# Kernel tuning notes

Hardware: AMD Instinct MI355X
Metric: run time of the kernel (lower is better)

The kernel has to match this reference:

```python
import jax, jax.numpy as jnp
import numpy as np

# Static problem sizes (uniform complexes so the per-complex torch loop vectorizes)
B, P, L = 8, 512, 64          # complexes, protein atoms/complex, ligand atoms/complex
H, RB = 128, 32               # hidden_dim, radial_bins
CUTOFF = 8.0
NPT, NLT = 20, 16             # atom-type vocab sizes


def _linear_init(k, din, dout):
    s = 1.0 / np.sqrt(din)
    kw, kb = jax.random.split(k)
    W = jax.random.uniform(kw, (din, dout), minval=-s, maxval=s, dtype=jnp.float32)
    b = jax.random.uniform(kb, (dout,), minval=-s, maxval=s, dtype=jnp.float32)
    return W, b


def setup_inputs() -> dict:
    key = jax.random.key(0)
    ks = jax.random.split(key, 12)
    # positions spread over ~a pocket-sized box so the cutoff mask is non-trivial
    protein_pos = jax.random.normal(ks[0], (B * P, 3), dtype=jnp.float32) * 4.0
    ligand_pos = jax.random.normal(ks[1], (B * L, 3), dtype=jnp.float32) * 4.0
    protein_atom_type = jax.random.randint(ks[2], (B * P,), 0, NPT)
    ligand_atom_type = jax.random.randint(ks[3], (B * L,), 0, NLT)
    protein_batch = jnp.repeat(jnp.arange(B), P)
    ligand_batch = jnp.repeat(jnp.arange(B), L)
    prot_emb = jax.random.normal(ks[4], (NPT, H), dtype=jnp.float32)
    lig_emb = jax.random.normal(ks[5], (NLT, H), dtype=jnp.float32)
    W1, b1 = _linear_init(ks[6], 2 * H + RB, H)
    W2, b2 = _linear_init(ks[7], H, H)
    W3, b3 = _linear_init(ks[8], H, H)
    Wr1, br1 = _linear_init(ks[9], H, H)
    Wr2, br2 = _linear_init(ks[10], H, 1)
    return dict(protein_pos=protein_pos, ligand_pos=ligand_pos,
                prot_emb=prot_emb, lig_emb=lig_emb,
                W1=W1, b1=b1, W2=W2, b2=b2, W3=W3, b3=b3,
                Wr1=Wr1, br1=br1, Wr2=Wr2, br2=br2,
                protein_atom_type=protein_atom_type, ligand_atom_type=ligand_atom_type,
                protein_batch=protein_batch, ligand_batch=ligand_batch)


def reference(protein_pos, ligand_pos, prot_emb, lig_emb,
              W1, b1, W2, b2, W3, b3, Wr1, br1, Wr2, br2,
              protein_atom_type, ligand_atom_type, protein_batch, ligand_batch):
    # batches are contiguous with uniform P/L atoms per complex -> reshape to [B, ., .]
    pos_p = protein_pos.reshape(B, P, 3)
    pos_l = ligand_pos.reshape(B, L, 3)
    hp = prot_emb[protein_atom_type].reshape(B, P, H)
    hl = lig_emb[ligand_atom_type].reshape(B, L, H)

    diff = pos_p[:, :, None, :] - pos_l[:, None, :, :]          # [B,P,L,3]
    dist = jnp.linalg.norm(diff, axis=-1)                        # [B,P,L]
    mask = dist < CUTOFF                                         # [B,P,L]

    centers = jnp.linspace(0.0, CUTOFF, RB, dtype=dist.dtype)    # radial_centers buffer
    width = jnp.asarray(0.5 * CUTOFF / RB, dtype=dist.dtype)     # radial_width buffer
    rb = jnp.exp(-0.5 * ((dist[..., None] - centers) / (width + 1e-8)) ** 2)  # [B,P,L,RB]

    pair = jnp.concatenate([
        jnp.broadcast_to(hp[:, :, None, :], (B, P, L, H)),
        jnp.broadcast_to(hl[:, None, :, :], (B, P, L, H)),
        rb,
    ], axis=-1)                                                  # [B,P,L,2H+RB]

    h = jax.nn.relu(pair @ W1 + b1)
    h = jax.nn.relu(h @ W2 + b2)
    h = jax.nn.relu(h @ W3 + b3)                                 # [B,P,L,H]

    m = mask[..., None].astype(h.dtype)
    cnt = jnp.sum(mask, axis=(1, 2)).astype(h.dtype)             # valid pairs per complex
    complex_repr = jnp.sum(h * m, axis=(1, 2)) / jnp.maximum(cnt, 1.0)[:, None]  # [B,H]

    score = jax.nn.relu(complex_repr @ Wr1 + br1) @ Wr2 + br2    # [B,1]
    score = jnp.where(cnt[:, None] > 0, score, 0.0)              # torch emits 0 if no pairs
    return score[:, 0]                                           # [B]
```

## Files before the change

kernel.cpp:

```cpp
#include <hip/hip_runtime.h>
#include <hip/hip_bf16.h>
#include <math.h>

#define NB 8
#define NP 512
#define NL 64
#define NH 128
#define NRB 32
#define NPT 20
#define NLT 16
#define PAIRS_CAP (NP * NL)
#define CHUNKS 512
#define K1 96

typedef __attribute__((ext_vector_type(8))) _Float16 h8;
typedef __attribute__((ext_vector_type(4))) float f4;

__global__ __launch_bounds__(128) void build_tables(
    const float* __restrict__ pemb, const float* __restrict__ lemb,
    const float* __restrict__ W1, const float* __restrict__ b1,
    float* __restrict__ tp, float* __restrict__ tl,
    float* __restrict__ acc)
{
  int blk = blockIdx.x, tid = threadIdx.x;
  if (blk == NPT + NLT) {
    for (int i = tid; i < NB * NH; i += 128) acc[i] = 0.0f;
    return;
  }
  __shared__ float se[NH];
  bool isP = (blk < NPT);
  int t = isP ? blk : (blk - NPT);
  const float* emb = isP ? (pemb + t * NH) : (lemb + t * NH);
  se[tid] = emb[tid];
  __syncthreads();
  int off = isP ? 0 : NH;
  float s = isP ? b1[tid] : 0.0f;
  for (int k = 0; k < NH; ++k)
    s = fmaf(se[k], W1[(off + k) * NH + tid], s);
  if (isP) tp[t * NH + tid] = s;
  else     tl[t * NH + tid] = s;
}

__global__ __launch_bounds__(128) void pack_weights(
    const float* __restrict__ W1, const float* __restrict__ W2,
    const float* __restrict__ W3,
    const float* __restrict__ tp, const float* __restrict__ tl,
    _Float16* __restrict__ wt1e, _Float16* __restrict__ wt2t,
    _Float16* __restrict__ wt3t)
{
  int k = blockIdx.x, c = threadIdx.x;
  wt2t[c * NH + k] = (_Float16)W2[k * NH + c];
  wt3t[c * NH + k] = (_Float16)W3[k * NH + c];
  if (k < K1) {
    float v;
    if (k < 32)      v = W1[(2 * NH + k) * NH + c];
    else if (k < 52) v = tp[(k - 32) * NH + c];
    else if (k < 68) v = tl[(k - 52) * NH + c];
    else             v = 0.0f;
    wt1e[c * K1 + k] = (_Float16)v;
  }
}

__global__ __launch_bounds__(256) void compact_pairs(
    const float* __restrict__ ppos, const float* __restrict__ lpos,
    unsigned short* __restrict__ wl, unsigned* __restrict__ cnt)
{
  int b = blockIdx.x;
  int tid = threadIdx.x;
  int w = tid >> 6, lane = tid & 63;
  __shared__ float slig[NL * 3];
  __shared__ unsigned wtot[4];

  if (tid < NL * 3) slig[tid] = lpos[b * NL * 3 + tid];
  __syncthreads();

  const float* pp = ppos + (size_t)(b * NP + 2 * tid) * 3;
  float p0x = pp[0], p0y = pp[1], p0z = pp[2];
  float p1x = pp[3], p1y = pp[4], p1z = pp[5];

  unsigned long long m0 = 0ull, m1 = 0ull;
  for (int l = 0; l < NL; ++l) {
    float qx = slig[3 * l + 0], qy = slig[3 * l + 1], qz = slig[3 * l + 2];
    float dx0 = p0x - qx, dy0 = p0y - qy, dz0 = p0z - qz;
    float dx1 = p1x - qx, dy1 = p1y - qy, dz1 = p1z - qz;
    bool v0 = sqrtf(dx0 * dx0 + dy0 * dy0 + dz0 * dz0) < 8.0f;
    bool v1 = sqrtf(dx1 * dx1 + dy1 * dy1 + dz1 * dz1) < 8.0f;
    m0 |= ((unsigned long long)v0) << l;
    m1 |= ((unsigned long long)v1) << l;
  }
  unsigned count = (unsigned)(__popcll(m0) + __popcll(m1));

  unsigned inc = count;
  #pragma unroll
  for (int d = 1; d < 64; d <<= 1) {
    unsigned v = __shfl_up(inc, d);
    if (lane >= d) inc += v;
  }
  if (lane == 63) wtot[w] = inc;
  __syncthreads();
  unsigned wbase = 0;
  for (int i = 0; i < w; ++i) wbase += wtot[i];
  unsigned base = wbase + inc - count;
  if (tid == 255) cnt[b] = wbase + inc;

  unsigned short* dst = wl + b * PAIRS_CAP;
  unsigned pb0 = (unsigned)(2 * tid) << 6, pb1 = pb0 + 64u;
  unsigned long long mm = m0;
  while (mm) {
    int l = __builtin_ctzll(mm); mm &= mm - 1ull;
    dst[base++] = (unsigned short)(pb0 | (unsigned)l);
  }
  mm = m1;
  while (mm) {
    int l = __builtin_ctzll(mm); mm &= mm - 1ull;
    dst[base++] = (unsigned short)(pb1 | (unsigned)l);
  }
}

__device__ __forceinline__ int swz(int row, int col) {
  return row * NH + (col ^ ((row & 7) << 3));
}

__global__ __launch_bounds__(256, 4) void pair_mlp(
    const float* __restrict__ ppos, const float* __restrict__ lpos,
    const int* __restrict__ ptype_g, const int* __restrict__ ltype_g,
    const _Float16* __restrict__ wt1e, const _Float16* __restrict__ wt2t,
    const _Float16* __restrict__ wt3t,
    const float* __restrict__ b2, const float* __restrict__ b3,
    const unsigned short* __restrict__ wl, const unsigned* __restrict__ cnt,
    float* __restrict__ accum)
{
  __shared__ _Float16 sA[NL * NH];
  __shared__ _Float16 sB[NL * NH];

  int tid = threadIdx.x;
  int cg = __builtin_amdgcn_readfirstlane(tid >> 6);
  int l  = tid & 63;
  int b     = blockIdx.x & 7;
  int chunk = blockIdx.x >> 3;

  unsigned total = cnt[b];
  if ((unsigned)(chunk * 64) >= total) return;

  int idx = chunk * 64 + l;
  int src = ((unsigned)idx < total) ? idx : 0;
  int pr = (int)wl[b * PAIRS_CAP + src];
  int p = pr >> 6, li = pr & 63;
  int gp = b * NP + p, gl = b * NL + li;

  float px = ppos[gp * 3 + 0], py = ppos[gp * 3 + 1], pz = ppos[gp * 3 + 2];
  float qx = lpos[gl * 3 + 0], qy = lpos[gl * 3 + 1], qz = lpos[gl * 3 + 2];
  int pt = ptype_g[gp], lt = ltype_g[gl];

  float dx = px - qx, dy = py - qy, dz = pz - qz;
  float dist = sqrtf(dx * dx + dy * dy + dz * dz);
  const float stepc = 8.0f / 31.0f;
  const float invw = 1.0f / (0.125f + 1e-8f);

  for (int jj = 0; jj < 3; ++jj) {
    int ch = 3 * cg + jj;
    h8 v;
    #pragma unroll
    for (int i = 0; i < 8; ++i) {
      int c = ch * 8 + i;
      float x;
      if (c < 32) { float t = (dist - stepc * (float)c) * invw; x = __expf(-0.5f * t * t); }
      else if (c < 52) x = (c - 32 == pt) ? 1.0f : 0.0f;
      else if (c < 68) x = (c - 52 == lt) ? 1.0f : 0.0f;
      else x = 0.0f;
      v[i] = (_Float16)x;
    }
    *(h8*)&sB[swz(l, ch * 8)] = v;
  }
  __syncthreads();

  int col0 = cg * 32 + (l & 15);
  int krow = 8 * (l >> 4);
  int g4 = (l >> 4) * 4;

  {
    h8 B1[2][3];
    #pragma unroll
    for (int n = 0; n < 2; ++n)
      #pragma unroll
      for (int kk = 0; kk < 3; ++kk)
        B1[n][kk] = *(const h8*)&wt1e[(col0 + 16 * n) * K1 + 32 * kk + krow];

    f4 acc1[4][2];
    #pragma unroll
    for (int m = 0; m < 4; ++m)
      #pragma unroll
      for (int n = 0; n < 2; ++n)
        acc1[m][n] = (f4){0.0f, 0.0f, 0.0f, 0.0f};

    #pragma unroll
    for (int m = 0; m < 4; ++m) {
      int row = 16 * m + (l & 15);
      #pragma unroll
      for (int kk = 0; kk < 3; ++kk) {
        h8 a = *(const h8*)&sB[swz(row, 32 * kk + krow)];
        acc1[m][0] = __builtin_amdgcn_mfma_f32_16x16x32_f16(a, B1[0][kk], acc1[m][0], 0, 0, 0);
        acc1[m][1] = __builtin_amdgcn_mfma_f32_16x16x32_f16(a, B1[1][kk], acc1[m][1], 0, 0, 0);
      }
    }
    #pragma unroll
    for (int m = 0; m < 4; ++m)
      #pragma unroll
      for (int n = 0; n < 2; ++n)
        #pragma unroll
        for (int r = 0; r < 4; ++r) {
          int row = 16 * m + g4 + r;
          sA[swz(row, cg * 32 + 16 * n + (l & 15))] =
              (_Float16)fmaxf(acc1[m][n][r], 0.0f);
        }
  }
  __syncthreads();

  {
    h8 B2[2][4];
    #pragma unroll
    for (int n = 0; n < 2; ++n)
      #pragma unroll
      for (int kk = 0; kk < 4; ++kk)
        B2[n][kk] = *(const h8*)&wt2t[(col0 + 16 * n) * NH + 32 * kk + krow];

    float bias0 = b2[col0], bias1 = b2[col0 + 16];
    f4 acc2[4][2];
    #pragma unroll
    for (int m = 0; m < 4; ++m) {
      acc2[m][0] = (f4){bias0, bias0, bias0, bias0};
      acc2[m][1] = (f4){bias1, bias1, bias1, bias1};
    }
    #pragma unroll
    for (int m = 0; m < 4; ++m) {
      int row = 16 * m + (l & 15);
      #pragma unroll
      for (int kk = 0; kk < 4; ++kk) {
        h8 a = *(const h8*)&sA[swz(row, 32 * kk + krow)];
        acc2[m][0] = __builtin_amdgcn_mfma_f32_16x16x32_f16(a, B2[0][kk], acc2[m][0], 0, 0, 0);
        acc2[m][1] = __builtin_amdgcn_mfma_f32_16x16x32_f16(a, B2[1][kk], acc2[m][1], 0, 0, 0);
      }
    }
    __syncthreads();
    #pragma unroll
    for (int m = 0; m < 4; ++m)
      #pragma unroll
      for (int n = 0; n < 2; ++n)
        #pragma unroll
        for (int r = 0; r < 4; ++r) {
          int row = 16 * m + g4 + r;
          sB[swz(row, cg * 32 + 16 * n + (l & 15))] =
              (_Float16)fmaxf(acc2[m][n][r], 0.0f);
        }
  }
  __syncthreads();

  {
    h8 B3[2][4];
    #pragma unroll
    for (int n = 0; n < 2; ++n)
      #pragma unroll
      for (int kk = 0; kk < 4; ++kk)
        B3[n][kk] = *(const h8*)&wt3t[(col0 + 16 * n) * NH + 32 * kk + krow];

    float bias0 = b3[col0], bias1 = b3[col0 + 16];
    f4 acc3[4][2];
    #pragma unroll
    for (int m = 0; m < 4; ++m) {
      acc3[m][0] = (f4){bias0, bias0, bias0, bias0};
      acc3[m][1] = (f4){bias1, bias1, bias1, bias1};
    }
    #pragma unroll
    for (int m = 0; m < 4; ++m) {
      int row = 16 * m + (l & 15);
      #pragma unroll
      for (int kk = 0; kk < 4; ++kk) {
        h8 a = *(const h8*)&sB[swz(row, 32 * kk + krow)];
        acc3[m][0] = __builtin_amdgcn_mfma_f32_16x16x32_f16(a, B3[0][kk], acc3[m][0], 0, 0, 0);
        acc3[m][1] = __builtin_amdgcn_mfma_f32_16x16x32_f16(a, B3[1][kk], acc3[m][1], 0, 0, 0);
      }
    }

    int rem = (int)total - chunk * 64;
    float cs0 = 0.0f, cs1 = 0.0f;
    #pragma unroll
    for (int m = 0; m < 4; ++m)
      #pragma unroll
      for (int r = 0; r < 4; ++r) {
        int row = 16 * m + g4 + r;
        bool ok = row < rem;
        cs0 += ok ? fmaxf(acc3[m][0][r], 0.0f) : 0.0f;
        cs1 += ok ? fmaxf(acc3[m][1][r], 0.0f) : 0.0f;
      }
    cs0 += __shfl_xor(cs0, 16); cs0 += __shfl_xor(cs0, 32);
    cs1 += __shfl_xor(cs1, 16); cs1 += __shfl_xor(cs1, 32);
    int g = l >> 4;
    if (g == 0)      atomicAdd(&accum[b * NH + cg * 32 + (l & 15)], cs0);
    else if (g == 1) atomicAdd(&accum[b * NH + cg * 32 + 16 + (l & 15)], cs1);
  }
}

__global__ __launch_bounds__(128) void score_head(
    const float* __restrict__ acc, const unsigned* __restrict__ cnt,
    const float* __restrict__ Wr1, const float* __restrict__ br1,
    const float* __restrict__ Wr2, const float* __restrict__ br2,
    float* __restrict__ out)
{
  int b = blockIdx.x;
  int tid = threadIdx.x;
  __shared__ float sr[NH];
  __shared__ float sv[NH];
  unsigned c = cnt[b];
  float denom = fmaxf((float)c, 1.0f);
  sr[tid] = acc[b * NH + tid] / denom;
  __syncthreads();
  float s = br1[tid];
  for (int k = 0; k < NH; ++k)
    s = fmaf(sr[k], Wr1[k * NH + tid], s);
  sv[tid] = fmaxf(s, 0.0f) * Wr2[tid];
  __syncthreads();
  if (tid == 0) {
    float sc = br2[0];
    for (int k = 0; k < NH; ++k) sc += sv[k];
    out[b] = (c > 0) ? sc : 0.0f;
  }
}

extern "C" void kernel_launch(void* const* d_in, const int* in_sizes, int n_in,
                              void* d_out, int out_size, void* d_ws, size_t ws_size,
                              hipStream_t stream)
{
  const float* ppos = (const float*)d_in[0];
  const float* lpos = (const float*)d_in[1];
  const float* pemb = (const float*)d_in[2];
  const float* lemb = (const float*)d_in[3];
  const float* W1   = (const float*)d_in[4];
  const float* b1   = (const float*)d_in[5];
  const float* W2   = (const float*)d_in[6];
  const float* b2   = (const float*)d_in[7];
  const float* W3   = (const float*)d_in[8];
  const float* b3   = (const float*)d_in[9];
  const float* Wr1  = (const float*)d_in[10];
  const float* br1  = (const float*)d_in[11];
  const float* Wr2  = (const float*)d_in[12];
  const float* br2  = (const float*)d_in[13];
  const int*   ptyp = (const int*)d_in[14];
  const int*   ltyp = (const int*)d_in[15];

  float* ws  = (float*)d_ws;
  float* tp  = ws;
  float* tl  = ws + 2560;
  float* acc = ws + 4608;
  unsigned* cnt = (unsigned*)(ws + 5632);
  unsigned short* wl = (unsigned short*)(ws + 5648);
  _Float16* wt1e = (_Float16*)(ws + 5648 + 131072);
  _Float16* wt2t = (_Float16*)(ws + 5648 + 131072 + 6144);
  _Float16* wt3t = (_Float16*)(ws + 5648 + 131072 + 6144 + 8192);

  build_tables<<<NPT + NLT + 1, 128, 0, stream>>>(pemb, lemb, W1, b1, tp, tl, acc);
  pack_weights<<<NH, NH, 0, stream>>>(W1, W2, W3, tp, tl, wt1e, wt2t, wt3t);
  compact_pairs<<<NB, 256, 0, stream>>>(ppos, lpos, wl, cnt);
  pair_mlp<<<NB * CHUNKS, 256, 0, stream>>>(ppos, lpos, ptyp, ltyp,
                                            wt1e, wt2t, wt3t, b2, b3,
                                            wl, cnt, acc);
  score_head<<<NB, 128, 0, stream>>>(acc, cnt, Wr1, br1, Wr2, br2, (float*)d_out);
}
```

Baseline: 54.96 us.

## Merge prep kernels into one launch and process two chunks per MLP block

The table-building, weight-packing and pair-compaction kernels are folded into one prep kernel with role-dispatched blocks. The embedding-times-W1 tables are now computed inline per packed column, which removes the intermediate tp/tl buffers. The goal is to cut two kernel launches and their serialization gaps. The pair MLP now handles two 64-pair chunks per block in a loop, halving the grid and launch overhead but serializing work within each block. The prep blocks that compute embedding tables redo a 128-long dot product per thread, and each such block writes a strided column.

```diff
diff --git a/kernel.cpp b/kernel.cpp
--- a/kernel.cpp
+++ b/kernel.cpp
@@ -11,109 +11,114 @@
 #define NLT 16
 #define PAIRS_CAP (NP * NL)
 #define CHUNKS 512
+#define CPB 2
 #define K1 96
 
 typedef __attribute__((ext_vector_type(8))) _Float16 h8;
 typedef __attribute__((ext_vector_type(4))) float f4;
 
-__global__ __launch_bounds__(128) void build_tables(
+__global__ __launch_bounds__(256) void prep(
+    const float* __restrict__ ppos, const float* __restrict__ lpos,
     const float* __restrict__ pemb, const float* __restrict__ lemb,
     const float* __restrict__ W1, const float* __restrict__ b1,
-    float* __restrict__ tp, float* __restrict__ tl,
-    float* __restrict__ acc)
+    const float* __restrict__ W2, const float* __restrict__ W3,
+    unsigned short* __restrict__ wl, unsigned* __restrict__ cnt,
+    _Float16* __restrict__ wt1e, _Float16* __restrict__ wt2t,
+    _Float16* __restrict__ wt3t, float* __restrict__ acc)
 {
   int blk = blockIdx.x, tid = threadIdx.x;
-  if (blk == NPT + NLT) {
-    for (int i = tid; i < NB * NH; i += 128) acc[i] = 0.0f;
+
+  if (blk < 8) {
+    int b = blk;
+    int w = tid >> 6, lane = tid & 63;
+    __shared__ float slig[NL * 3];
+    __shared__ unsigned wtot[4];
+
+    if (tid < NL * 3) slig[tid] = lpos[b * NL * 3 + tid];
+    __syncthreads();
+
+    const float* pp = ppos + (size_t)(b * NP + 2 * tid) * 3;
+    float p0x = pp[0], p0y = pp[1], p0z = pp[2];
+    float p1x = pp[3], p1y = pp[4], p1z = pp[5];
+
+    unsigned long long m0 = 0ull, m1 = 0ull;
+    for (int l = 0; l < NL; ++l) {
+      float qx = slig[3 * l + 0], qy = slig[3 * l + 1], qz = slig[3 * l + 2];
+      float dx0 = p0x - qx, dy0 = p0y - qy, dz0 = p0z - qz;
+      float dx1 = p1x - qx, dy1 = p1y - qy, dz1 = p1z - qz;
+      bool v0 = sqrtf(dx0 * dx0 + dy0 * dy0 + dz0 * dz0) < 8.0f;
+      bool v1 = sqrtf(dx1 * dx1 + dy1 * dy1 + dz1 * dz1) < 8.0f;
+      m0 |= ((unsigned long long)v0) << l;
+      m1 |= ((unsigned long long)v1) << l;
+    }
+    unsigned count = (unsigned)(__popcll(m0) + __popcll(m1));
+
+    unsigned inc = count;
+    #pragma unroll
+    for (int d = 1; d < 64; d <<= 1) {
+      unsigned v = __shfl_up(inc, d);
+      if (lane >= d) inc += v;
+    }
+    if (lane == 63) wtot[w] = inc;
+    __syncthreads();
+    unsigned wbase = 0;
+    for (int i = 0; i < w; ++i) wbase += wtot[i];
+    unsigned base = wbase + inc - count;
+    if (tid == 255) cnt[b] = wbase + inc;
+
+    unsigned short* dst = wl + b * PAIRS_CAP;
+    unsigned pb0 = (unsigned)(2 * tid) << 6, pb1 = pb0 + 64u;
+    unsigned long long mm = m0;
+    while (mm) {
+      int l = __builtin_ctzll(mm); mm &= mm - 1ull;
+      dst[base++] = (unsigned short)(pb0 | (unsigned)l);
+    }
+    mm = m1;
+    while (mm) {
+      int l = __builtin_ctzll(mm); mm &= mm - 1ull;
+      dst[base++] = (unsigned short)(pb1 | (unsigned)l);
+    }
     return;
   }
-  __shared__ float se[NH];
-  bool isP = (blk < NPT);
-  int t = isP ? blk : (blk - NPT);
-  const float* emb = isP ? (pemb + t * NH) : (lemb + t * NH);
-  se[tid] = emb[tid];
-  __syncthreads();
-  int off = isP ? 0 : NH;
-  float s = isP ? b1[tid] : 0.0f;
-  for (int k = 0; k < NH; ++k)
-    s = fmaf(se[k], W1[(off + k) * NH + tid], s);
-  if (isP) tp[t * NH + tid] = s;
-  else     tl[t * NH + tid] = s;
-}
-
-__global__ __launch_bounds__(128) void pack_weights(
-    const float* __restrict__ W1, const float* __restrict__ W2,
-    const float* __restrict__ W3,
-    const float* __restrict__ tp, const float* __restrict__ tl,
-    _Float16* __restrict__ wt1e, _Float16* __restrict__ wt2t,
-    _Float16* __restrict__ wt3t)
-{
-  int k = blockIdx.x, c = threadIdx.x;
-  wt2t[c * NH + k] = (_Float16)W2[k * NH + c];
-  wt3t[c * NH + k] = (_Float16)W3[k * NH + c];
-  if (k < K1) {
+
+  if (blk == 8) {
+    for (int i = tid; i < NB * NH; i += 256) acc[i] = 0.0f;
+    return;
+  }
+
+  if (blk < 105) {
+    int k = blk - 9;
+    if (tid >= NH) return;
+    int c = tid;
     float v;
-    if (k < 32)      v = W1[(2 * NH + k) * NH + c];
-    else if (k < 52) v = tp[(k - 32) * NH + c];
-    else if (k < 68) v = tl[(k - 52) * NH + c];
-    else             v = 0.0f;
+    if (k < 32) {
+      v = W1[(2 * NH + k) * NH + c];
+    } else if (k < 52) {
+      int t = k - 32;
+      float s = b1[c];
+      for (int j = 0; j < NH; ++j)
+        s = fmaf(pemb[t * NH + j], W1[j * NH + c], s);
+      v = s;
+    } else if (k < 68) {
+      int t = k - 52;
+      float s = 0.0f;
+      for (int j = 0; j < NH; ++j)
+        s = fmaf(lemb[t * NH + j], W1[(NH + j) * NH + c], s);
+      v = s;
+    } else {
+      v = 0.0f;
+    }
     wt1e[c * K1 + k] = (_Float16)v;
-  }
-}
-
-__global__ __launch_bounds__(256) void compact_pairs(
-    const float* __restrict__ ppos, const float* __restrict__ lpos,
-    unsigned short* __restrict__ wl, unsigned* __restrict__ cnt)
-{
-  int b = blockIdx.x;
-  int tid = threadIdx.x;
-  int w = tid >> 6, lane = tid & 63;
-  __shared__ float slig[NL * 3];
-  __shared__ unsigned wtot[4];
-
-  if (tid < NL * 3) slig[tid] = lpos[b * NL * 3 + tid];
-  __syncthreads();
-
-  const float* pp = ppos + (size_t)(b * NP + 2 * tid) * 3;
-  float p0x = pp[0], p0y = pp[1], p0z = pp[2];
-  float p1x = pp[3], p1y = pp[4], p1z = pp[5];
-
-  unsigned long long m0 = 0ull, m1 = 0ull;
-  for (int l = 0; l < NL; ++l) {
-    float qx = slig[3 * l + 0], qy = slig[3 * l + 1], qz = slig[3 * l + 2];
-    float dx0 = p0x - qx, dy0 = p0y - qy, dz0 = p0z - qz;
-    float dx1 = p1x - qx, dy1 = p1y - qy, dz1 = p1z - qz;
-    bool v0 = sqrtf(dx0 * dx0 + dy0 * dy0 + dz0 * dz0) < 8.0f;
-    bool v1 = sqrtf(dx1 * dx1 + dy1 * dy1 + dz1 * dz1) < 8.0f;
-    m0 |= ((unsigned long long)v0) << l;
-    m1 |= ((unsigned long long)v1) << l;
-  }
-  unsigned count = (unsigned)(__popcll(m0) + __popcll(m1));
-
-  unsigned inc = count;
-  #pragma unroll
-  for (int d = 1; d < 64; d <<= 1) {
-    unsigned v = __shfl_up(inc, d);
-    if (lane >= d) inc += v;
-  }
-  if (lane == 63) wtot[w] = inc;
-  __syncthreads();
-  unsigned wbase = 0;
-  for (int i = 0; i < w; ++i) wbase += wtot[i];
-  unsigned base = wbase + inc - count;
-  if (tid == 255) cnt[b] = wbase + inc;
-
-  unsigned short* dst = wl + b * PAIRS_CAP;
-  unsigned pb0 = (unsigned)(2 * tid) << 6, pb1 = pb0 + 64u;
-  unsigned long long mm = m0;
-  while (mm) {
-    int l = __builtin_ctzll(mm); mm &= mm - 1ull;
-    dst[base++] = (unsigned short)(pb0 | (unsigned)l);
-  }
-  mm = m1;
-  while (mm) {
-    int l = __builtin_ctzll(mm); mm &= mm - 1ull;
-    dst[base++] = (unsigned short)(pb1 | (unsigned)l);
+    return;
+  }
+
+  {
+    int k = blk - 105;
+    if (tid >= NH) return;
+    int c = tid;
+    wt2t[c * NH + k] = (_Float16)W2[k * NH + c];
+    wt3t[c * NH + k] = (_Float16)W3[k * NH + c];
+    return;
   }
 }
 
@@ -136,167 +141,173 @@
   int tid = threadIdx.x;
   int cg = __builtin_amdgcn_readfirstlane(tid >> 6);
   int l  = tid & 63;
-  int b     = blockIdx.x & 7;
-  int chunk = blockIdx.x >> 3;
+  int b   = blockIdx.x & 7;
+  int cb  = (blockIdx.x >> 3) * CPB;
 
   unsigned total = cnt[b];
-  if ((unsigned)(chunk * 64) >= total) return;
-
-  int idx = chunk * 64 + l;
-  int src = ((unsigned)idx < total) ? idx : 0;
-  int pr = (int)wl[b * PAIRS_CAP + src];
-  int p = pr >> 6, li = pr & 63;
-  int gp = b * NP + p, gl = b * NL + li;
-
-  float px = ppos[gp * 3 + 0], py = ppos[gp * 3 + 1], pz = ppos[gp * 3 + 2];
-  float qx = lpos[gl * 3 + 0], qy = lpos[gl * 3 + 1], qz = lpos[gl * 3 + 2];
-  int pt = ptype_g[gp], lt = ltype_g[gl];
-
-  float dx = px - qx, dy = py - qy, dz = pz - qz;
-  float dist = sqrtf(dx * dx + dy * dy + dz * dz);
-  const float stepc = 8.0f / 31.0f;
-  const float invw = 1.0f / (0.125f + 1e-8f);
-
-  for (int jj = 0; jj < 3; ++jj) {
-    int ch = 3 * cg + jj;
-    h8 v;
-    #pragma unroll
-    for (int i = 0; i < 8; ++i) {
-      int c = ch * 8 + i;
-      float x;
-      if (c < 32) { float t = (dist - stepc * (float)c) * invw; x = __expf(-0.5f * t * t); }
-      else if (c < 52) x = (c - 32 == pt) ? 1.0f : 0.0f;
-      else if (c < 68) x = (c - 52 == lt) ? 1.0f : 0.0f;
-      else x = 0.0f;
-      v[i] = (_Float16)x;
-    }
-    *(h8*)&sB[swz(l, ch * 8)] = v;
-  }
-  __syncthreads();
+  if ((unsigned)(cb * 64) >= total) return;
 
   int col0 = cg * 32 + (l & 15);
   int krow = 8 * (l >> 4);
   int g4 = (l >> 4) * 4;
-
-  {
-    h8 B1[2][3];
-    #pragma unroll
-    for (int n = 0; n < 2; ++n)
-      #pragma unroll
-      for (int kk = 0; kk < 3; ++kk)
-        B1[n][kk] = *(const h8*)&wt1e[(col0 + 16 * n) * K1 + 32 * kk + krow];
-
-    f4 acc1[4][2];
-    #pragma unroll
-    for (int m = 0; m < 4; ++m)
+  const float stepc = 8.0f / 31.0f;
+  const float invw = 1.0f / (0.125f + 1e-8f);
+
+  for (int cc = 0; cc < CPB; ++cc) {
+    int chunk = cb + cc;
+    if ((unsigned)(chunk * 64) >= total) break;
+    if (cc) __syncthreads();
+
+    int idx = chunk * 64 + l;
+    int src = ((unsigned)idx < total) ? idx : 0;
+    int pr = (int)wl[b * PAIRS_CAP + src];
+    int p = pr >> 6, li = pr & 63;
+    int gp = b * NP + p, gl = b * NL + li;
+
+    float px = ppos[gp * 3 + 0], py = ppos[gp * 3 + 1], pz = ppos[gp * 3 + 2];
+    float qx = lpos[gl * 3 + 0], qy = lpos[gl * 3 + 1], qz = lpos[gl * 3 + 2];
+    int pt = ptype_g[gp], lt = ltype_g[gl];
+
+    float dx = px - qx, dy = py - qy, dz = pz - qz;
+    float dist = sqrtf(dx * dx + dy * dy + dz * dz);
+
+    for (int jj = 0; jj < 3; ++jj) {
+      int ch = 3 * cg + jj;
+      h8 v;
+      #pragma unroll
+      for (int i = 0; i < 8; ++i) {
+        int c = ch * 8 + i;
+        float x;
+        if (c < 32) { float t = (dist - stepc * (float)c) * invw; x = __expf(-0.5f * t * t); }
+        else if (c < 52) x = (c - 32 == pt) ? 1.0f : 0.0f;
+        else if (c < 68) x = (c - 52 == lt) ? 1.0f : 0.0f;
+        else x = 0.0f;
+        v[i] = (_Float16)x;
+      }
+      *(h8*)&sB[swz(l, ch * 8)] = v;
+    }
+    __syncthreads();
+
+    {
+      h8 B1[2][3];
       #pragma unroll
       for (int n = 0; n < 2; ++n)
-        acc1[m][n] = (f4){0.0f, 0.0f, 0.0f, 0.0f};
-
-    #pragma unroll
-    for (int m = 0; m < 4; ++m) {
-      int row = 16 * m + (l & 15);
-      #pragma unroll
-      for (int kk = 0; kk < 3; ++kk) {
-        h8 a = *(const h8*)&sB[swz(row, 32 * kk + krow)];
-        acc1[m][0] = __builtin_amdgcn_mfma_f32_16x16x32_f16(a, B1[0][kk], acc1[m][0], 0, 0, 0);
-        acc1[m][1] = __builtin_amdgcn_mfma_f32_16x16x32_f16(a, B1[1][kk], acc1[m][1], 0, 0, 0);
-      }
-    }
-    #pragma unroll
-    for (int m = 0; m < 4; ++m)
+        #pragma unroll
+        for (int kk = 0; kk < 3; ++kk)
+          B1[n][kk] = *(const h8*)&wt1e[(col0 + 16 * n) * K1 + 32 * kk + krow];
+
+      f4 acc1[4][2];
+      #pragma unroll
+      for (int m = 0; m < 4; ++m)
+        #pragma unroll
+        for (int n = 0; n < 2; ++n)
+          acc1[m][n] = (f4){0.0f, 0.0f, 0.0f, 0.0f};
+
+      #pragma unroll
+      for (int m = 0; m < 4; ++m) {
+        int row = 16 * m + (l & 15);
+        #pragma unroll
+        for (int kk = 0; kk < 3; ++kk) {
+          h8 a = *(const h8*)&sB[swz(row, 32 * kk + krow)];
+          acc1[m][0] = __builtin_amdgcn_mfma_f32_16x16x32_f16(a, B1[0][kk], acc1[m][0], 0, 0, 0);
+          acc1[m][1] = __builtin_amdgcn_mfma_f32_16x16x32_f16(a, B1[1][kk], acc1[m][1], 0, 0, 0);
+        }
+      }
+      #pragma unroll
+      for (int m = 0; m < 4; ++m)
+        #pragma unroll
+        for (int n = 0; n < 2; ++n)
+          #pragma unroll
+          for (int r = 0; r < 4; ++r) {
+            int row = 16 * m + g4 + r;
+            sA[swz(row, cg * 32 + 16 * n + (l & 15))] =
+                (_Float16)fmaxf(acc1[m][n][r], 0.0f);
+          }
+    }
+    __syncthreads();
+
+    {
+      h8 B2[2][4];
       #pragma unroll
       for (int n = 0; n < 2; ++n)
+        #pragma unroll
+        for (int kk = 0; kk < 4; ++kk)
+          B2[n][kk] = *(const h8*)&wt2t[(col0 + 16 * n) * NH + 32 * kk + krow];
+
+      float bias0 = b2[col0], bias1 = b2[col0 + 16];
+      f4 acc2[4][2];
+      #pragma unroll
+      for (int m = 0; m < 4; ++m) {
+        acc2[m][0] = (f4){bias0, bias0, bias0, bias0};
+        acc2[m][1] = (f4){bias1, bias1, bias1, bias1};
+      }
+      #pragma unroll
+      for (int m = 0; m < 4; ++m) {
+        int row = 16 * m + (l & 15);
+        #pragma unroll
+        for (int kk = 0; kk < 4; ++kk) {
+          h8 a = *(const h8*)&sA[swz(row, 32 * kk + krow)];
+          acc2[m][0] = __builtin_amdgcn_mfma_f32_16x16x32_f16(a, B2[0][kk], acc2[m][0], 0, 0, 0);
+          acc2[m][1] = __builtin_amdgcn_mfma_f32_16x16x32_f16(a, B2[1][kk], acc2[m][1], 0, 0, 0);
+        }
+      }
+      __syncthreads();
+      #pragma unroll
+      for (int m = 0; m < 4; ++m)
+        #pragma unroll
+        for (int n = 0; n < 2; ++n)
+          #pragma unroll
+          for (int r = 0; r < 4; ++r) {
+            int row = 16 * m + g4 + r;
+            sB[swz(row, cg * 32 + 16 * n + (l & 15))] =
+                (_Float16)fmaxf(acc2[m][n][r], 0.0f);
+          }
+    }
+    __syncthreads();
+
+    {
+      h8 B3[2][4];
+      #pragma unroll
+      for (int n = 0; n < 2; ++n)
+        #pragma unroll
+        for (int kk = 0; kk < 4; ++kk)
+          B3[n][kk] = *(const h8*)&wt3t[(col0 + 16 * n) * NH + 32 * kk + krow];
+
+      float bias0 = b3[col0], bias1 = b3[col0 + 16];
+      f4 acc3[4][2];
+      #pragma unroll
+      for (int m = 0; m < 4; ++m) {
+        acc3[m][0] = (f4){bias0, bias0, bias0, bias0};
+        acc3[m][1] = (f4){bias1, bias1, bias1, bias1};
+      }
+      #pragma unroll
+      for (int m = 0; m < 4; ++m) {
+        int row = 16 * m + (l & 15);
+        #pragma unroll
+        for (int kk = 0; kk < 4; ++kk) {
+          h8 a = *(const h8*)&sB[swz(row, 32 * kk + krow)];
+          acc3[m][0] = __builtin_amdgcn_mfma_f32_16x16x32_f16(a, B3[0][kk], acc3[m][0], 0, 0, 0);
+          acc3[m][1] = __builtin_amdgcn_mfma_f32_16x16x32_f16(a, B3[1][kk], acc3[m][1], 0, 0, 0);
+        }
+      }
+
+      int rem = (int)total - chunk * 64;
+      float cs0 = 0.0f, cs1 = 0.0f;
+      #pragma unroll
+      for (int m = 0; m < 4; ++m)
         #pragma unroll
         for (int r = 0; r < 4; ++r) {
           int row = 16 * m + g4 + r;
-          sA[swz(row, cg * 32 + 16 * n + (l & 15))] =
-              (_Float16)fmaxf(acc1[m][n][r], 0.0f);
+          bool ok = row < rem;
+          cs0 += ok ? fmaxf(acc3[m][0][r], 0.0f) : 0.0f;
+          cs1 += ok ? fmaxf(acc3[m][1][r], 0.0f) : 0.0f;
         }
-  }
-  __syncthreads();
-
-  {
-    h8 B2[2][4];
-    #pragma unroll
-    for (int n = 0; n < 2; ++n)
-      #pragma unroll
-      for (int kk = 0; kk < 4; ++kk)
-        B2[n][kk] = *(const h8*)&wt2t[(col0 + 16 * n) * NH + 32 * kk + krow];
-
-    float bias0 = b2[col0], bias1 = b2[col0 + 16];
-    f4 acc2[4][2];
-    #pragma unroll
-    for (int m = 0; m < 4; ++m) {
-      acc2[m][0] = (f4){bias0, bias0, bias0, bias0};
-      acc2[m][1] = (f4){bias1, bias1, bias1, bias1};
-    }
-    #pragma unroll
-    for (int m = 0; m < 4; ++m) {
-      int row = 16 * m + (l & 15);
-      #pragma unroll
-      for (int kk = 0; kk < 4; ++kk) {
-        h8 a = *(const h8*)&sA[swz(row, 32 * kk + krow)];
-        acc2[m][0] = __builtin_amdgcn_mfma_f32_16x16x32_f16(a, B2[0][kk], acc2[m][0], 0, 0, 0);
-        acc2[m][1] = __builtin_amdgcn_mfma_f32_16x16x32_f16(a, B2[1][kk], acc2[m][1], 0, 0, 0);
-      }
-    }
-    __syncthreads();
-    #pragma unroll
-    for (int m = 0; m < 4; ++m)
-      #pragma unroll
-      for (int n = 0; n < 2; ++n)
-        #pragma unroll
-        for (int r = 0; r < 4; ++r) {
-          int row = 16 * m + g4 + r;
-          sB[swz(row, cg * 32 + 16 * n + (l & 15))] =
-              (_Float16)fmaxf(acc2[m][n][r], 0.0f);
-        }
-  }
-  __syncthreads();
-
-  {
-    h8 B3[2][4];
-    #pragma unroll
-    for (int n = 0; n < 2; ++n)
-      #pragma unroll
-      for (int kk = 0; kk < 4; ++kk)
-        B3[n][kk] = *(const h8*)&wt3t[(col0 + 16 * n) * NH + 32 * kk + krow];
-
-    float bias0 = b3[col0], bias1 = b3[col0 + 16];
-    f4 acc3[4][2];
-    #pragma unroll
-    for (int m = 0; m < 4; ++m) {
-      acc3[m][0] = (f4){bias0, bias0, bias0, bias0};
-      acc3[m][1] = (f4){bias1, bias1, bias1, bias1};
-    }
-    #pragma unroll
-    for (int m = 0; m < 4; ++m) {
-      int row = 16 * m + (l & 15);
-      #pragma unroll
-      for (int kk = 0; kk < 4; ++kk) {
-        h8 a = *(const h8*)&sB[swz(row, 32 * kk + krow)];
-        acc3[m][0] = __builtin_amdgcn_mfma_f32_16x16x32_f16(a, B3[0][kk], acc3[m][0], 0, 0, 0);
-        acc3[m][1] = __builtin_amdgcn_mfma_f32_16x16x32_f16(a, B3[1][kk], acc3[m][1], 0, 0, 0);
-      }
-    }
-
-    int rem = (int)total - chunk * 64;
-    float cs0 = 0.0f, cs1 = 0.0f;
-    #pragma unroll
-    for (int m = 0; m < 4; ++m)
-      #pragma unroll
-      for (int r = 0; r < 4; ++r) {
-        int row = 16 * m + g4 + r;
-        bool ok = row < rem;
-        cs0 += ok ? fmaxf(acc3[m][0][r], 0.0f) : 0.0f;
-        cs1 += ok ? fmaxf(acc3[m][1][r], 0.0f) : 0.0f;
-      }
-    cs0 += __shfl_xor(cs0, 16); cs0 += __shfl_xor(cs0, 32);
-    cs1 += __shfl_xor(cs1, 16); cs1 += __shfl_xor(cs1, 32);
-    int g = l >> 4;
-    if (g == 0)      atomicAdd(&accum[b * NH + cg * 32 + (l & 15)], cs0);
-    else if (g == 1) atomicAdd(&accum[b * NH + cg * 32 + 16 + (l & 15)], cs1);
+      cs0 += __shfl_xor(cs0, 16); cs0 += __shfl_xor(cs0, 32);
+      cs1 += __shfl_xor(cs1, 16); cs1 += __shfl_xor(cs1, 32);
+      int g = l >> 4;
+      if (g == 0)      atomicAdd(&accum[b * NH + cg * 32 + (l & 15)], cs0);
+      else if (g == 1) atomicAdd(&accum[b * NH + cg * 32 + 16 + (l & 15)], cs1);
+    }
   }
 }
 
@@ -348,8 +359,6 @@
   const int*   ltyp = (const int*)d_in[15];
 
   float* ws  = (float*)d_ws;
-  float* tp  = ws;
-  float* tl  = ws + 2560;
   float* acc = ws + 4608;
   unsigned* cnt = (unsigned*)(ws + 5632);
   unsigned short* wl = (unsigned short*)(ws + 5648);
@@ -357,11 +366,10 @@
   _Float16* wt2t = (_Float16*)(ws + 5648 + 131072 + 6144);
   _Float16* wt3t = (_Float16*)(ws + 5648 + 131072 + 6144 + 8192);
 
-  build_tables<<<NPT + NLT + 1, 128, 0, stream>>>(pemb, lemb, W1, b1, tp, tl, acc);
-  pack_weights<<<NH, NH, 0, stream>>>(W1, W2, W3, tp, tl, wt1e, wt2t, wt3t);
-  compact_pairs<<<NB, 256, 0, stream>>>(ppos, lpos, wl, cnt);
-  pair_mlp<<<NB * CHUNKS, 256, 0, stream>>>(ppos, lpos, ptyp, ltyp,
-                                            wt1e, wt2t, wt3t, b2, b3,
-                                            wl, cnt, acc);
+  prep<<<233, 256, 0, stream>>>(ppos, lpos, pemb, lemb, W1, b1, W2, W3,
+                                wl, cnt, wt1e, wt2t, wt3t, acc);
+  pair_mlp<<<NB * (CHUNKS / CPB), 256, 0, stream>>>(ppos, lpos, ptyp, ltyp,
+                                                    wt1e, wt2t, wt3t, b2, b3,
+                                                    wl, cnt, acc);
   score_head<<<NB, 128, 0, stream>>>(acc, cnt, Wr1, br1, Wr2, br2, (float*)d_out);
 }
```

Result: slower. 78.70 us (+43.2%).
